# Performance work log

Measured on AMD Instinct MI355X. Metric: run time of the kernel, lower is better.

## Reference

```python
import jax, jax.numpy as jnp
import numpy as np

NB = 8  # num_blocks

def setup_inputs() -> dict:
    key = jax.random.key(0)
    ks = jax.random.split(key, 8)
    C = 128
    C8 = C // 8
    s = 0.05
    x = jax.random.normal(ks[0], (1, C, 64, 64, 64), dtype=jnp.float32)
    Wq = jax.random.normal(ks[1], (C8, C), dtype=jnp.float32) * s
    bq = jax.random.normal(ks[2], (C8,), dtype=jnp.float32) * s
    Wk = jax.random.normal(ks[3], (C8, C), dtype=jnp.float32) * s
    bk = jax.random.normal(ks[4], (C8,), dtype=jnp.float32) * s
    Wv = jax.random.normal(ks[5], (C, C), dtype=jnp.float32) * s
    bv = jax.random.normal(ks[6], (C,), dtype=jnp.float32) * s
    # torch inits gamma=0 (output == x, zero grads through attention);
    # use 0.5 so the attention path is actually exercised.
    gamma = jnp.full((1,), 0.5, dtype=jnp.float32)
    return dict(x=x, Wq=Wq, bq=bq, Wk=Wk, bk=bk, Wv=Wv, bv=bv, gamma=gamma)

def reference(x, Wq, bq, Wk, bk, Wv, bv, gamma):
    B, C, D, H, W = x.shape
    db, hb, wb = D // NB, H // NB, W // NB
    n = db * hb * wb
    # (i, j, k, B, C, db, hb, wb) block layout
    xr = x.reshape(B, C, NB, db, NB, hb, NB, wb).transpose(2, 4, 6, 0, 1, 3, 5, 7)
    ar = jnp.arange(NB)
    # NOTE: original code computes k = i % num_blocks, i.e. k == i always.
    # Only the (i, j, i) diagonal blocks are attended; the rest stay zero in `out`.
    blk = xr[ar, :, ar].reshape(NB * NB * B, C, n)  # (P, C, n), P = NB*NB*B
    # 1x1x1 convs == per-voxel linear layers over channels
    q = jnp.einsum('pcn,dc->pdn', blk, Wq) + bq[None, :, None]  # (P, C/8, n)
    k = jnp.einsum('pcn,dc->pdn', blk, Wk) + bk[None, :, None]  # (P, C/8, n)
    v = jnp.einsum('pcn,dc->pdn', blk, Wv) + bv[None, :, None]  # (P, C,   n)
    attn = jax.nn.softmax(jnp.einsum('pdn,pdm->pnm', q, k), axis=-1)  # (P, n_q, n_k)
    ob = jnp.einsum('pdm,pnm->pdn', v, attn)  # value @ attn^T, (P, C, n)
    ob = ob.reshape(NB, NB, B, C, db, hb, wb)
    out = jnp.zeros_like(xr).at[ar, :, ar].set(ob)  # only k==i diagonal filled
    out = out.transpose(3, 4, 0, 5, 1, 6, 2, 7).reshape(B, C, D, H, W)
    return gamma * out + x
```

## Files before the change

### kernel.cpp

```cpp
#include <hip/hip_runtime.h>

typedef __attribute__((ext_vector_type(8))) short bf16x8;
typedef __attribute__((ext_vector_type(4))) float f32x4;
typedef __attribute__((ext_vector_type(4))) int i32x4;
typedef __attribute__((ext_vector_type(4))) float float4v;

#define MFMA16(a, b, c) __builtin_amdgcn_mfma_f32_16x16x32_bf16((a), (b), (c), 0, 0, 0)

__device__ __forceinline__ unsigned short f2bf(float f) {
    unsigned u = __builtin_bit_cast(unsigned, f);
    u += 0x7fffu + ((u >> 16) & 1u);
    return (unsigned short)(u >> 16);
}
__device__ __forceinline__ float bf2f(unsigned short s) {
    unsigned u = ((unsigned)s) << 16;
    return __builtin_bit_cast(float, u);
}
__device__ __forceinline__ int pkbf(float a, float b) {
    return (int)f2bf(a) | ((int)f2bf(b) << 16);
}

#define KOFF 131072
#define LOFF 147456

__global__ __launch_bounds__(512, 2) void battn_kernel(
    const float* __restrict__ x,
    const float* __restrict__ Wq, const float* __restrict__ bq,
    const float* __restrict__ Wk, const float* __restrict__ bk,
    const float* __restrict__ Wv, const float* __restrict__ bv,
    const float* __restrict__ gamma, float* __restrict__ out)
{
    __shared__ __attribute__((aligned(128))) char smem[147968];
    const int tid = threadIdx.x;
    const int bid = blockIdx.x;
    const int p  = ((bid & 7) << 3) | (bid >> 5);
    const int qq = (bid >> 3) & 3;
    const int ib = p >> 3, jb = p & 7;
    const int vbase = ib * 8 * 4096 + jb * 8 * 64 + ib * 8;
    const int lane = tid & 63, wv = tid >> 6;
    const int g = lane >> 4, c15 = lane & 15;

    #pragma unroll
    for (int b = 0; b < 4; ++b) {
        float4v t[8];
        #pragma unroll
        for (int j = 0; j < 8; ++j) {
            int ch = (b * 8 + j) * 512 + tid;
            int c = ch >> 7;
            int m = (ch & 127) * 4;
            int vox = ((m >> 6) << 12) + (((m >> 3) & 7) << 6) + (m & 7);
            t[j] = *(const float4v*)(x + c * 262144 + vbase + vox);
        }
        #pragma unroll
        for (int j = 0; j < 8; ++j) {
            int ch = (b * 8 + j) * 512 + tid;
            int c = ch >> 7;
            int m = (ch & 127) * 4;
            char* bp = smem + ((m * 256 + 2 * c) ^ (((m >> 2) & 7) << 4));
            *(unsigned short*)(bp)       = f2bf(t[j][0]);
            *(unsigned short*)(bp + 256) = f2bf(t[j][1]);
            *(unsigned short*)(bp + 512) = f2bf(t[j][2]);
            *(unsigned short*)(bp + 768) = f2bf(t[j][3]);
        }
    }

    bf16x8 wqf[4], wkf[4], wvf[4];
    #pragma unroll
    for (int ks = 0; ks < 4; ++ks) {
        const float4v* sq = (const float4v*)(Wq + c15 * 128 + ks * 32 + g * 8);
        const float4v* sk = (const float4v*)(Wk + c15 * 128 + ks * 32 + g * 8);
        const float4v* sv = (const float4v*)(Wv + (wv * 16 + c15) * 128 + ks * 32 + g * 8);
        float4v q0 = sq[0], q1 = sq[1];
        float4v k0 = sk[0], k1 = sk[1];
        float4v v0 = sv[0], v1 = sv[1];
        #pragma unroll
        for (int e = 0; e < 4; ++e) {
            wqf[ks][e] = (short)f2bf(q0[e]); wqf[ks][4 + e] = (short)f2bf(q1[e]);
            wkf[ks][e] = (short)f2bf(k0[e]); wkf[ks][4 + e] = (short)f2bf(k1[e]);
            wvf[ks][e] = (short)f2bf(v0[e]); wvf[ks][4 + e] = (short)f2bf(v1[e]);
        }
    }
    const float bqv = bq[c15], bkv = bk[c15];
    const f32x4 zacc = {0.f, 0.f, 0.f, 0.f};
    const bf16x8 zfrag = (bf16x8)(short)0;

    __syncthreads();

    {
        f32x4 acc = zacc;
        int mrow = qq * 128 + wv * 16 + c15;
        int sw = ((mrow >> 2) & 7) << 4;
        #pragma unroll
        for (int ks = 0; ks < 4; ++ks) {
            bf16x8 af = *(const bf16x8*)(smem + ((mrow * 256 + ks * 64 + g * 16) ^ sw));
            acc = MFMA16(af, wqf[ks], acc);
        }
        #pragma unroll
        for (int r = 0; r < 4; ++r)
            *(unsigned short*)(smem + KOFF + wv * 2048 + (g * 4 + r) * 32 + 2 * c15) = f2bf(acc[r] + bqv);
    }
    bf16x8 qf = zfrag;
    if (g < 2) qf = *(const bf16x8*)(smem + KOFF + wv * 2048 + c15 * 32 + g * 16);

    #pragma unroll
    for (int qi = 0; qi < 4; ++qi) {
        f32x4 acc = zacc;
        int mrow = wv * 64 + qi * 16 + c15;
        int sw = ((mrow >> 2) & 7) << 4;
        #pragma unroll
        for (int ks = 0; ks < 4; ++ks) {
            bf16x8 af = *(const bf16x8*)(smem + ((mrow * 256 + ks * 64 + g * 16) ^ sw));
            acc = MFMA16(af, wkf[ks], acc);
        }
        #pragma unroll
        for (int r = 0; r < 4; ++r) {
            int mk = wv * 64 + qi * 16 + g * 4 + r;
            *(unsigned short*)(smem + KOFF + mk * 32 + 2 * c15) = f2bf(acc[r] + bkv);
        }
    }

    for (int ck = 0; ck < 4; ++ck) {
        f32x4 vacc[8];
        #pragma unroll
        for (int mt = 0; mt < 8; ++mt) {
            vacc[mt] = zacc;
            int mrow = ck * 128 + mt * 16 + c15;
            int sw = ((mrow >> 2) & 7) << 4;
            #pragma unroll
            for (int ks = 0; ks < 4; ++ks) {
                bf16x8 bf = *(const bf16x8*)(smem + ((mrow * 256 + ks * 64 + g * 16) ^ sw));
                vacc[mt] = MFMA16(wvf[ks], bf, vacc[mt]);
            }
        }
        __syncthreads();
        #pragma unroll
        for (int mt = 0; mt < 8; ++mt) {
            #pragma unroll
            for (int r = 0; r < 4; ++r) {
                int c_out = wv * 16 + g * 4 + r;
                int mkl = mt * 16 + c15;
                *(unsigned short*)(smem + ck * 32768 + c_out * 256 +
                                   ((2 * mkl) ^ ((c_out & 7) << 4))) = f2bf(vacc[mt][r]);
            }
        }
    }
    __syncthreads();

    f32x4 o[8];
    #pragma unroll
    for (int ci = 0; ci < 8; ++ci) o[ci] = zacc;
    float lsum = 0.f;

    for (int kt = 0; kt < 16; ++kt) {
        int mk0 = kt * 32;
        bf16x8 ka[2];
        #pragma unroll
        for (int ki = 0; ki < 2; ++ki) {
            bf16x8 v = zfrag;
            if (g < 2) v = *(const bf16x8*)(smem + KOFF + (mk0 + ki * 16 + c15) * 32 + g * 16);
            ka[ki] = v;
        }

        f32x4 s0 = MFMA16(ka[0], qf, zacc);
        f32x4 s1 = MFMA16(ka[1], qf, zacc);
        float e00 = __expf(s0[0]), e01 = __expf(s0[1]), e02 = __expf(s0[2]), e03 = __expf(s0[3]);
        float e10 = __expf(s1[0]), e11 = __expf(s1[1]), e12 = __expf(s1[2]), e13 = __expf(s1[3]);
        lsum += (e00 + e01) + (e02 + e03) + ((e10 + e11) + (e12 + e13));
        int wA0 = pkbf(e00, e01), wB0 = pkbf(e02, e03);
        int wA1 = pkbf(e10, e11), wB1 = pkbf(e12, e13);
        int src1 = ((2 * g) & 3) * 16 + c15;
        int src2 = ((2 * g + 1) & 3) * 16 + c15;
        int sA0a = __shfl(wA0, src1, 64), sA1a = __shfl(wA1, src1, 64);
        int sB0a = __shfl(wB0, src1, 64), sB1a = __shfl(wB1, src1, 64);
        int sA0b = __shfl(wA0, src2, 64), sA1b = __shfl(wA1, src2, 64);
        int sB0b = __shfl(wB0, src2, 64), sB1b = __shfl(wB1, src2, 64);
        bool k1 = (g >= 2);
        i32x4 uu = { k1 ? sA1a : sA0a, k1 ? sB1a : sB0a,
                     k1 ? sA1b : sA0b, k1 ? sB1b : sB0b };
        bf16x8 pa = __builtin_bit_cast(bf16x8, uu);

        int ckbase = (mk0 >> 7) * 32768;
        int mklb = (2 * (mk0 & 127)) + 16 * g;
        #pragma unroll
        for (int ci = 0; ci < 8; ++ci) {
            int c = ci * 16 + c15;
            bf16x8 vb = *(const bf16x8*)(smem + ckbase + c * 256 + (mklb ^ ((c & 7) << 4)));
            o[ci] = MFMA16(pa, vb, o[ci]);
        }
    }

    {
        float l = lsum;
        l += __shfl_xor(l, 16, 64);
        l += __shfl_xor(l, 32, 64);
        if (g == 0)
            *(float*)(smem + LOFF + (wv * 16 + c15) * 4) = l;
    }

    __syncthreads();

    #pragma unroll
    for (int ci = 0; ci < 8; ++ci)
        #pragma unroll
        for (int r = 0; r < 4; ++r) {
            int nql = wv * 16 + g * 4 + r;
            int c = ci * 16 + c15;
            *(unsigned short*)(smem + c * 256 + ((2 * nql) ^ ((c & 7) << 4))) = f2bf(o[ci][r]);
        }
    __syncthreads();

    float gma = gamma[0];
    int q128 = tid & 127;
    int cb = tid >> 7;
    float invl = 1.0f / *(const float*)(smem + LOFF + q128 * 4);
    int nq = qq * 128 + q128;
    int vox = ((nq >> 6) << 12) + (((nq >> 3) & 7) << 6) + (nq & 7);
    int go = vbase + vox;
    #pragma unroll
    for (int b = 0; b < 4; ++b) {
        float xv[8];
        #pragma unroll
        for (int j = 0; j < 8; ++j) {
            int c = cb * 32 + b * 8 + j;
            xv[j] = out[c * 262144 + go];
        }
        #pragma unroll
        for (int j = 0; j < 8; ++j) {
            int c = cb * 32 + b * 8 + j;
            float ov = bf2f(*(const unsigned short*)(smem + c * 256 + ((2 * q128) ^ ((c & 7) << 4))));
            out[c * 262144 + go] = gma * (ov * invl + bv[c]) + xv[j];
        }
    }
}

extern "C" void kernel_launch(void* const* d_in, const int* in_sizes, int n_in,
                              void* d_out, int out_size, void* d_ws, size_t ws_size,
                              hipStream_t stream) {
    const float* x     = (const float*)d_in[0];
    const float* Wq    = (const float*)d_in[1];
    const float* bq    = (const float*)d_in[2];
    const float* Wk    = (const float*)d_in[3];
    const float* bk    = (const float*)d_in[4];
    const float* Wv    = (const float*)d_in[5];
    const float* bv    = (const float*)d_in[6];
    const float* gamma = (const float*)d_in[7];
    float* out = (float*)d_out;
    (void)in_sizes; (void)n_in; (void)out_size; (void)d_ws; (void)ws_size;

    hipMemcpyAsync(out, x, (size_t)out_size * sizeof(float),
                   hipMemcpyDeviceToDevice, stream);
    battn_kernel<<<dim3(256), dim3(512), 0, stream>>>(x, Wq, bq, Wk, bk, Wv, bv, gamma, out);
}
```

Before: 101.6 us.

## Add dedicated epilogue warps that prefetch residual while compute warps run attention

Doubles the block to 1024 threads, with 8 extra waves that help load x into shared memory. Those waves then prefetch the residual output values into registers while the original 8 waves run the QKV projections and the attention loop. Afterwards the extra waves perform the final gamma-scaled write. The aim is to overlap global residual loads with MFMA compute. In exchange it uses more registers per thread (32 prefetched floats), runs one block per CU, and relies on barrier counts matching across divergent branches.

```diff
diff --git a/kernel.cpp b/kernel.cpp
--- a/kernel.cpp
+++ b/kernel.cpp
@@ -23,7 +23,7 @@
 #define KOFF 131072
 #define LOFF 147456
 
-__global__ __launch_bounds__(512, 2) void battn_kernel(
+__global__ __launch_bounds__(1024, 1) void battn_kernel(
     const float* __restrict__ x,
     const float* __restrict__ Wq, const float* __restrict__ bq,
     const float* __restrict__ Wk, const float* __restrict__ bk,
@@ -39,13 +39,15 @@
     const int vbase = ib * 8 * 4096 + jb * 8 * 64 + ib * 8;
     const int lane = tid & 63, wv = tid >> 6;
     const int g = lane >> 4, c15 = lane & 15;
+    const f32x4 zacc = {0.f, 0.f, 0.f, 0.f};
+    const bf16x8 zfrag = (bf16x8)(short)0;
 
     #pragma unroll
-    for (int b = 0; b < 4; ++b) {
+    for (int b = 0; b < 2; ++b) {
         float4v t[8];
         #pragma unroll
         for (int j = 0; j < 8; ++j) {
-            int ch = (b * 8 + j) * 512 + tid;
+            int ch = (b * 8 + j) * 1024 + tid;
             int c = ch >> 7;
             int m = (ch & 127) * 4;
             int vox = ((m >> 6) << 12) + (((m >> 3) & 7) << 6) + (m & 7);
@@ -53,7 +55,7 @@
         }
         #pragma unroll
         for (int j = 0; j < 8; ++j) {
-            int ch = (b * 8 + j) * 512 + tid;
+            int ch = (b * 8 + j) * 1024 + tid;
             int c = ch >> 7;
             int m = (ch & 127) * 4;
             char* bp = smem + ((m * 256 + 2 * c) ^ (((m >> 2) & 7) << 4));
@@ -65,170 +67,191 @@
     }
 
     bf16x8 wqf[4], wkf[4], wvf[4];
-    #pragma unroll
-    for (int ks = 0; ks < 4; ++ks) {
-        const float4v* sq = (const float4v*)(Wq + c15 * 128 + ks * 32 + g * 8);
-        const float4v* sk = (const float4v*)(Wk + c15 * 128 + ks * 32 + g * 8);
-        const float4v* sv = (const float4v*)(Wv + (wv * 16 + c15) * 128 + ks * 32 + g * 8);
-        float4v q0 = sq[0], q1 = sq[1];
-        float4v k0 = sk[0], k1 = sk[1];
-        float4v v0 = sv[0], v1 = sv[1];
-        #pragma unroll
-        for (int e = 0; e < 4; ++e) {
-            wqf[ks][e] = (short)f2bf(q0[e]); wqf[ks][4 + e] = (short)f2bf(q1[e]);
-            wkf[ks][e] = (short)f2bf(k0[e]); wkf[ks][4 + e] = (short)f2bf(k1[e]);
-            wvf[ks][e] = (short)f2bf(v0[e]); wvf[ks][4 + e] = (short)f2bf(v1[e]);
-        }
-    }
-    const float bqv = bq[c15], bkv = bk[c15];
-    const f32x4 zacc = {0.f, 0.f, 0.f, 0.f};
-    const bf16x8 zfrag = (bf16x8)(short)0;
+    float bqv = 0.f, bkv = 0.f;
+    if (wv < 8) {
+        #pragma unroll
+        for (int ks = 0; ks < 4; ++ks) {
+            const float4v* sq = (const float4v*)(Wq + c15 * 128 + ks * 32 + g * 8);
+            const float4v* sk = (const float4v*)(Wk + c15 * 128 + ks * 32 + g * 8);
+            const float4v* sv = (const float4v*)(Wv + (wv * 16 + c15) * 128 + ks * 32 + g * 8);
+            float4v q0 = sq[0], q1 = sq[1];
+            float4v k0 = sk[0], k1 = sk[1];
+            float4v v0 = sv[0], v1 = sv[1];
+            #pragma unroll
+            for (int e = 0; e < 4; ++e) {
+                wqf[ks][e] = (short)f2bf(q0[e]); wqf[ks][4 + e] = (short)f2bf(q1[e]);
+                wkf[ks][e] = (short)f2bf(k0[e]); wkf[ks][4 + e] = (short)f2bf(k1[e]);
+                wvf[ks][e] = (short)f2bf(v0[e]); wvf[ks][4 + e] = (short)f2bf(v1[e]);
+            }
+        }
+        bqv = bq[c15]; bkv = bk[c15];
+    }
 
     __syncthreads();
 
-    {
-        f32x4 acc = zacc;
-        int mrow = qq * 128 + wv * 16 + c15;
-        int sw = ((mrow >> 2) & 7) << 4;
-        #pragma unroll
-        for (int ks = 0; ks < 4; ++ks) {
-            bf16x8 af = *(const bf16x8*)(smem + ((mrow * 256 + ks * 64 + g * 16) ^ sw));
-            acc = MFMA16(af, wqf[ks], acc);
-        }
-        #pragma unroll
-        for (int r = 0; r < 4; ++r)
-            *(unsigned short*)(smem + KOFF + wv * 2048 + (g * 4 + r) * 32 + 2 * c15) = f2bf(acc[r] + bqv);
-    }
     bf16x8 qf = zfrag;
-    if (g < 2) qf = *(const bf16x8*)(smem + KOFF + wv * 2048 + c15 * 32 + g * 16);
-
-    #pragma unroll
-    for (int qi = 0; qi < 4; ++qi) {
-        f32x4 acc = zacc;
-        int mrow = wv * 64 + qi * 16 + c15;
-        int sw = ((mrow >> 2) & 7) << 4;
-        #pragma unroll
-        for (int ks = 0; ks < 4; ++ks) {
-            bf16x8 af = *(const bf16x8*)(smem + ((mrow * 256 + ks * 64 + g * 16) ^ sw));
-            acc = MFMA16(af, wkf[ks], acc);
-        }
-        #pragma unroll
-        for (int r = 0; r < 4; ++r) {
-            int mk = wv * 64 + qi * 16 + g * 4 + r;
-            *(unsigned short*)(smem + KOFF + mk * 32 + 2 * c15) = f2bf(acc[r] + bkv);
+    if (wv < 8) {
+        {
+            f32x4 acc = zacc;
+            int mrow = qq * 128 + wv * 16 + c15;
+            int sw = ((mrow >> 2) & 7) << 4;
+            #pragma unroll
+            for (int ks = 0; ks < 4; ++ks) {
+                bf16x8 af = *(const bf16x8*)(smem + ((mrow * 256 + ks * 64 + g * 16) ^ sw));
+                acc = MFMA16(af, wqf[ks], acc);
+            }
+            #pragma unroll
+            for (int r = 0; r < 4; ++r)
+                *(unsigned short*)(smem + KOFF + wv * 2048 + (g * 4 + r) * 32 + 2 * c15) = f2bf(acc[r] + bqv);
+        }
+        if (g < 2) qf = *(const bf16x8*)(smem + KOFF + wv * 2048 + c15 * 32 + g * 16);
+
+        #pragma unroll
+        for (int qi = 0; qi < 4; ++qi) {
+            f32x4 acc = zacc;
+            int mrow = wv * 64 + qi * 16 + c15;
+            int sw = ((mrow >> 2) & 7) << 4;
+            #pragma unroll
+            for (int ks = 0; ks < 4; ++ks) {
+                bf16x8 af = *(const bf16x8*)(smem + ((mrow * 256 + ks * 64 + g * 16) ^ sw));
+                acc = MFMA16(af, wkf[ks], acc);
+            }
+            #pragma unroll
+            for (int r = 0; r < 4; ++r) {
+                int mk = wv * 64 + qi * 16 + g * 4 + r;
+                *(unsigned short*)(smem + KOFF + mk * 32 + 2 * c15) = f2bf(acc[r] + bkv);
+            }
         }
     }
 
     for (int ck = 0; ck < 4; ++ck) {
         f32x4 vacc[8];
-        #pragma unroll
-        for (int mt = 0; mt < 8; ++mt) {
-            vacc[mt] = zacc;
-            int mrow = ck * 128 + mt * 16 + c15;
-            int sw = ((mrow >> 2) & 7) << 4;
-            #pragma unroll
-            for (int ks = 0; ks < 4; ++ks) {
-                bf16x8 bf = *(const bf16x8*)(smem + ((mrow * 256 + ks * 64 + g * 16) ^ sw));
-                vacc[mt] = MFMA16(wvf[ks], bf, vacc[mt]);
-            }
-        }
-        __syncthreads();
-        #pragma unroll
-        for (int mt = 0; mt < 8; ++mt) {
+        if (wv < 8) {
+            #pragma unroll
+            for (int mt = 0; mt < 8; ++mt) {
+                vacc[mt] = zacc;
+                int mrow = ck * 128 + mt * 16 + c15;
+                int sw = ((mrow >> 2) & 7) << 4;
+                #pragma unroll
+                for (int ks = 0; ks < 4; ++ks) {
+                    bf16x8 bf = *(const bf16x8*)(smem + ((mrow * 256 + ks * 64 + g * 16) ^ sw));
+                    vacc[mt] = MFMA16(wvf[ks], bf, vacc[mt]);
+                }
+            }
+        }
+        __syncthreads();
+        if (wv < 8) {
+            #pragma unroll
+            for (int mt = 0; mt < 8; ++mt) {
+                #pragma unroll
+                for (int r = 0; r < 4; ++r) {
+                    int c_out = wv * 16 + g * 4 + r;
+                    int mkl = mt * 16 + c15;
+                    *(unsigned short*)(smem + ck * 32768 + c_out * 256 +
+                                       ((2 * mkl) ^ ((c_out & 7) << 4))) = f2bf(vacc[mt][r]);
+                }
+            }
+        }
+    }
+    __syncthreads();
+
+    float xv[32];
+    int go_e = 0;
+    float invl_dummy;
+    (void)invl_dummy;
+    if (wv >= 8) {
+        int t = tid - 512;
+        int q128 = t & 127;
+        int cb = t >> 7;
+        int nq = qq * 128 + q128;
+        int vox = ((nq >> 6) << 12) + (((nq >> 3) & 7) << 6) + (nq & 7);
+        go_e = vbase + vox;
+        #pragma unroll
+        for (int i = 0; i < 32; ++i) {
+            int c = cb * 32 + i;
+            xv[i] = out[c * 262144 + go_e];
+        }
+    }
+
+    if (wv < 8) {
+        f32x4 o[8];
+        #pragma unroll
+        for (int ci = 0; ci < 8; ++ci) o[ci] = zacc;
+        float lsum = 0.f;
+
+        for (int kt = 0; kt < 16; ++kt) {
+            int mk0 = kt * 32;
+            bf16x8 ka[2];
+            #pragma unroll
+            for (int ki = 0; ki < 2; ++ki) {
+                bf16x8 v = zfrag;
+                if (g < 2) v = *(const bf16x8*)(smem + KOFF + (mk0 + ki * 16 + c15) * 32 + g * 16);
+                ka[ki] = v;
+            }
+
+            f32x4 s0 = MFMA16(ka[0], qf, zacc);
+            f32x4 s1 = MFMA16(ka[1], qf, zacc);
+            float e00 = __expf(s0[0]), e01 = __expf(s0[1]), e02 = __expf(s0[2]), e03 = __expf(s0[3]);
+            float e10 = __expf(s1[0]), e11 = __expf(s1[1]), e12 = __expf(s1[2]), e13 = __expf(s1[3]);
+            lsum += (e00 + e01) + (e02 + e03) + ((e10 + e11) + (e12 + e13));
+            int wA0 = pkbf(e00, e01), wB0 = pkbf(e02, e03);
+            int wA1 = pkbf(e10, e11), wB1 = pkbf(e12, e13);
+            int src1 = ((2 * g) & 3) * 16 + c15;
+            int src2 = ((2 * g + 1) & 3) * 16 + c15;
+            int sA0a = __shfl(wA0, src1, 64), sA1a = __shfl(wA1, src1, 64);
+            int sB0a = __shfl(wB0, src1, 64), sB1a = __shfl(wB1, src1, 64);
+            int sA0b = __shfl(wA0, src2, 64), sA1b = __shfl(wA1, src2, 64);
+            int sB0b = __shfl(wB0, src2, 64), sB1b = __shfl(wB1, src2, 64);
+            bool k1 = (g >= 2);
+            i32x4 uu = { k1 ? sA1a : sA0a, k1 ? sB1a : sB0a,
+                         k1 ? sA1b : sA0b, k1 ? sB1b : sB0b };
+            bf16x8 pa = __builtin_bit_cast(bf16x8, uu);
+
+            int ckbase = (mk0 >> 7) * 32768;
+            int mklb = (2 * (mk0 & 127)) + 16 * g;
+            #pragma unroll
+            for (int ci = 0; ci < 8; ++ci) {
+                int c = ci * 16 + c15;
+                bf16x8 vb = *(const bf16x8*)(smem + ckbase + c * 256 + (mklb ^ ((c & 7) << 4)));
+                o[ci] = MFMA16(pa, vb, o[ci]);
+            }
+        }
+
+        {
+            float l = lsum;
+            l += __shfl_xor(l, 16, 64);
+            l += __shfl_xor(l, 32, 64);
+            if (g == 0)
+                *(float*)(smem + LOFF + (wv * 16 + c15) * 4) = l;
+        }
+
+        __syncthreads();
+
+        #pragma unroll
+        for (int ci = 0; ci < 8; ++ci)
             #pragma unroll
             for (int r = 0; r < 4; ++r) {
-                int c_out = wv * 16 + g * 4 + r;
-                int mkl = mt * 16 + c15;
-                *(unsigned short*)(smem + ck * 32768 + c_out * 256 +
-                                   ((2 * mkl) ^ ((c_out & 7) << 4))) = f2bf(vacc[mt][r]);
-            }
-        }
-    }
-    __syncthreads();
-
-    f32x4 o[8];
-    #pragma unroll
-    for (int ci = 0; ci < 8; ++ci) o[ci] = zacc;
-    float lsum = 0.f;
-
-    for (int kt = 0; kt < 16; ++kt) {
-        int mk0 = kt * 32;
-        bf16x8 ka[2];
-        #pragma unroll
-        for (int ki = 0; ki < 2; ++ki) {
-            bf16x8 v = zfrag;
-            if (g < 2) v = *(const bf16x8*)(smem + KOFF + (mk0 + ki * 16 + c15) * 32 + g * 16);
-            ka[ki] = v;
-        }
-
-        f32x4 s0 = MFMA16(ka[0], qf, zacc);
-        f32x4 s1 = MFMA16(ka[1], qf, zacc);
-        float e00 = __expf(s0[0]), e01 = __expf(s0[1]), e02 = __expf(s0[2]), e03 = __expf(s0[3]);
-        float e10 = __expf(s1[0]), e11 = __expf(s1[1]), e12 = __expf(s1[2]), e13 = __expf(s1[3]);
-        lsum += (e00 + e01) + (e02 + e03) + ((e10 + e11) + (e12 + e13));
-        int wA0 = pkbf(e00, e01), wB0 = pkbf(e02, e03);
-        int wA1 = pkbf(e10, e11), wB1 = pkbf(e12, e13);
-        int src1 = ((2 * g) & 3) * 16 + c15;
-        int src2 = ((2 * g + 1) & 3) * 16 + c15;
-        int sA0a = __shfl(wA0, src1, 64), sA1a = __shfl(wA1, src1, 64);
-        int sB0a = __shfl(wB0, src1, 64), sB1a = __shfl(wB1, src1, 64);
-        int sA0b = __shfl(wA0, src2, 64), sA1b = __shfl(wA1, src2, 64);
-        int sB0b = __shfl(wB0, src2, 64), sB1b = __shfl(wB1, src2, 64);
-        bool k1 = (g >= 2);
-        i32x4 uu = { k1 ? sA1a : sA0a, k1 ? sB1a : sB0a,
-                     k1 ? sA1b : sA0b, k1 ? sB1b : sB0b };
-        bf16x8 pa = __builtin_bit_cast(bf16x8, uu);
-
-        int ckbase = (mk0 >> 7) * 32768;
-        int mklb = (2 * (mk0 & 127)) + 16 * g;
-        #pragma unroll
-        for (int ci = 0; ci < 8; ++ci) {
-            int c = ci * 16 + c15;
-            bf16x8 vb = *(const bf16x8*)(smem + ckbase + c * 256 + (mklb ^ ((c & 7) << 4)));
-            o[ci] = MFMA16(pa, vb, o[ci]);
-        }
-    }
-
-    {
-        float l = lsum;
-        l += __shfl_xor(l, 16, 64);
-        l += __shfl_xor(l, 32, 64);
-        if (g == 0)
-            *(float*)(smem + LOFF + (wv * 16 + c15) * 4) = l;
-    }
-
-    __syncthreads();
-
-    #pragma unroll
-    for (int ci = 0; ci < 8; ++ci)
-        #pragma unroll
-        for (int r = 0; r < 4; ++r) {
-            int nql = wv * 16 + g * 4 + r;
-            int c = ci * 16 + c15;
-            *(unsigned short*)(smem + c * 256 + ((2 * nql) ^ ((c & 7) << 4))) = f2bf(o[ci][r]);
-        }
-    __syncthreads();
-
-    float gma = gamma[0];
-    int q128 = tid & 127;
-    int cb = tid >> 7;
-    float invl = 1.0f / *(const float*)(smem + LOFF + q128 * 4);
-    int nq = qq * 128 + q128;
-    int vox = ((nq >> 6) << 12) + (((nq >> 3) & 7) << 6) + (nq & 7);
-    int go = vbase + vox;
-    #pragma unroll
-    for (int b = 0; b < 4; ++b) {
-        float xv[8];
-        #pragma unroll
-        for (int j = 0; j < 8; ++j) {
-            int c = cb * 32 + b * 8 + j;
-            xv[j] = out[c * 262144 + go];
-        }
-        #pragma unroll
-        for (int j = 0; j < 8; ++j) {
-            int c = cb * 32 + b * 8 + j;
+                int nql = wv * 16 + g * 4 + r;
+                int c = ci * 16 + c15;
+                *(unsigned short*)(smem + c * 256 + ((2 * nql) ^ ((c & 7) << 4))) = f2bf(o[ci][r]);
+            }
+        __syncthreads();
+    } else {
+        __syncthreads();
+        __syncthreads();
+    }
+
+    if (wv >= 8) {
+        float gma = gamma[0];
+        int t = tid - 512;
+        int q128 = t & 127;
+        int cb = t >> 7;
+        float invl = 1.0f / *(const float*)(smem + LOFF + q128 * 4);
+        #pragma unroll
+        for (int i = 0; i < 32; ++i) {
+            int c = cb * 32 + i;
             float ov = bf2f(*(const unsigned short*)(smem + c * 256 + ((2 * q128) ^ ((c & 7) << 4))));
-            out[c * 262144 + go] = gma * (ov * invl + bv[c]) + xv[j];
+            out[c * 262144 + go_e] = gma * (ov * invl + bv[c]) + xv[i];
         }
     }
 }
@@ -249,5 +272,5 @@
 
     hipMemcpyAsync(out, x, (size_t)out_size * sizeof(float),
                    hipMemcpyDeviceToDevice, stream);
-    battn_kernel<<<dim3(256), dim3(512), 0, stream>>>(x, Wq, bq, Wk, bk, Wv, bv, gamma, out);
-}
+    battn_kernel<<<dim3(256), dim3(1024), 0, stream>>>(x, Wq, bq, Wk, bk, Wv, bv, gamma, out);
+}
```

Result: faster. 93.13 us (-8.4%).
